# Kernel optimization log

Measured on AMD Instinct MI355X. Metric: run time of the kernel, lower is better.

## Reference

```python
import jax, jax.numpy as jnp
import numpy as np

N_NODES = 20000
N_EDGES = 640000
NUM_FEATURES = 128
HIDDEN = 64
HEADS = 4
NUM_CLASSES = 16
NEG_SLOPE = 0.2  # PyG GATConv default leaky_relu slope


def gat_conv(x, src, dst, W, att_s, att_d, b, num_nodes, concat):
    """PyG-style GATConv (inference: attention dropout is identity).
    x: [N, F_in]; src/dst: [E] (self-loops already included);
    W: [F_in, H*C]; att_s/att_d: [H, C]; b: [H*C] or [C]."""
    H, C = att_s.shape
    h = (x @ W).reshape(num_nodes, H, C)            # [N,H,C]
    a_s = jnp.sum(h * att_s, axis=-1)               # [N,H]
    a_d = jnp.sum(h * att_d, axis=-1)               # [N,H]
    e = jax.nn.leaky_relu(a_s[src] + a_d[dst], NEG_SLOPE)  # [E,H]
    # softmax over incoming edges of each destination node
    emax = jax.ops.segment_max(e, dst, num_segments=num_nodes)  # [N,H]
    ex = jnp.exp(e - emax[dst])
    denom = jax.ops.segment_sum(ex, dst, num_segments=num_nodes)
    alpha = ex / denom[dst]                         # [E,H]
    msg = h[src] * alpha[..., None]                 # [E,H,C]
    out = jax.ops.segment_sum(msg, dst, num_segments=num_nodes)  # [N,H,C]
    out = out.reshape(num_nodes, H * C) if concat else out.mean(axis=1)
    return out + b


def setup_inputs() -> dict:
    key = jax.random.key(0)
    ks = jax.random.split(key, 12)
    d1_in, d1_out = NUM_FEATURES, HEADS * HIDDEN
    d2_in, d2_out = HEADS * HIDDEN, HEADS * HIDDEN
    return {
        "x": jax.random.normal(ks[0], (N_NODES, NUM_FEATURES), dtype=jnp.float32),
        "edge_index": jax.random.randint(ks[1], (2, N_EDGES), 0, N_NODES, dtype=jnp.int64)
        if jax.config.jax_enable_x64 else
        jax.random.randint(ks[1], (2, N_EDGES), 0, N_NODES, dtype=jnp.int32),
        "W1": jax.random.normal(ks[2], (d1_in, d1_out), dtype=jnp.float32) / np.sqrt(d1_in),
        "att_src1": jax.random.normal(ks[3], (HEADS, HIDDEN), dtype=jnp.float32) / np.sqrt(HIDDEN),
        "att_dst1": jax.random.normal(ks[4], (HEADS, HIDDEN), dtype=jnp.float32) / np.sqrt(HIDDEN),
        "b1": jnp.zeros((HEADS * HIDDEN,), dtype=jnp.float32),
        "W2": jax.random.normal(ks[5], (d2_in, d2_out), dtype=jnp.float32) / np.sqrt(d2_in),
        "att_src2": jax.random.normal(ks[6], (HEADS, HIDDEN), dtype=jnp.float32) / np.sqrt(HIDDEN),
        "att_dst2": jax.random.normal(ks[7], (HEADS, HIDDEN), dtype=jnp.float32) / np.sqrt(HIDDEN),
        "b2": jnp.zeros((HIDDEN,), dtype=jnp.float32),
        "Wout": jax.random.normal(ks[8], (HIDDEN, NUM_CLASSES), dtype=jnp.float32) / np.sqrt(HIDDEN),
        "bout": jnp.zeros((NUM_CLASSES,), dtype=jnp.float32),
    }


def reference(x, edge_index, W1, att_src1, att_dst1, b1, W2, att_src2, att_dst2, b2, Wout, bout):
    N = x.shape[0]
    loops = jnp.arange(N, dtype=edge_index.dtype)
    src = jnp.concatenate([edge_index[0], loops])   # PyG add_self_loops=True
    dst = jnp.concatenate([edge_index[1], loops])
    h = gat_conv(x, src, dst, W1, att_src1, att_dst1, b1, N, concat=True)
    h = jax.nn.elu(h)                               # dropout is identity at eval
    h = gat_conv(h, src, dst, W2, att_src2, att_dst2, b2, N, concat=False)
    return h @ Wout + bout
```

## Files before the change

### kernel.cpp

```cpp
#include <hip/hip_runtime.h>
#include <hip/hip_bf16.h>
#include <hip/hip_fp16.h>


#define HEADS 4
#define CDIM 64
#define HC 256
#define ELLW 96
#define CNTS 16
#define NCHUNK 320

typedef __attribute__((ext_vector_type(8))) short bf16x8;
typedef __attribute__((ext_vector_type(4))) float f32x4;

__device__ __forceinline__ short f32_to_bf16_rne(float v) {
  unsigned u = __float_as_uint(v);
  unsigned r = (u + 0x7FFFu + ((u >> 16) & 1u)) >> 16;
  return (short)r;
}
__device__ __forceinline__ float bf16_bits_to_f32(short s) {
  return __uint_as_float(((unsigned)(unsigned short)s) << 16);
}

__device__ __forceinline__ void fma_mix2(float& alo, float& ahi,
                                         unsigned reg, float ex) {
  asm("v_fma_mix_f32 %0, %2, %3, %0 op_sel:[0,0,0] op_sel_hi:[1,0,0]\n\t"
      "v_fma_mix_f32 %1, %2, %3, %1 op_sel:[1,0,0] op_sel_hi:[1,0,0]"
      : "+v"(alo), "+v"(ahi)
      : "v"(reg), "v"(ex));
}

__global__ __launch_bounds__(256) void pack_w12_kernel(
    const float* __restrict__ W1, short* __restrict__ W1h,
    short* __restrict__ W1l, const float* __restrict__ W2,
    short* __restrict__ W2h, short* __restrict__ W2l,
    int* __restrict__ cnt, int N) {
  const int i = blockIdx.x * 256 + threadIdx.x;
  if (i < N) cnt[i * CNTS] = 0;
  if (i < 128 * 256) {
    const int k = i >> 8, n = i & 255;
    const float v = W1[i];
    const short hi = f32_to_bf16_rne(v);
    W1h[n * 128 + k] = hi;
    W1l[n * 128 + k] = f32_to_bf16_rne(v - bf16_bits_to_f32(hi));
  } else {
    const int j = i - 128 * 256;
    if (j >= 256 * 256) return;
    const int k = j >> 8, n = j & 255;
    const float v = W2[j];
    const short hi = f32_to_bf16_rne(v);
    W2h[n * 256 + k] = hi;
    W2l[n * 256 + k] = f32_to_bf16_rne(v - bf16_bits_to_f32(hi));
  }
}

__global__ __launch_bounds__(128) void gemm_mfma_split(
    const float* __restrict__ A, const short* __restrict__ Wt_hi,
    const short* __restrict__ Wt_lo, __half* __restrict__ h16,
    const float* __restrict__ att_s, const float* __restrict__ att_d,
    float* __restrict__ a_s, float* __restrict__ a_d, int M, int K) {
  __shared__ alignas(16) short As_hi[64 * 32];
  __shared__ alignas(16) short As_lo[64 * 32];
  const int t = threadIdx.x;
  const int wave = t >> 6;
  const int lane = t & 63;
  const int quad = lane >> 4;
  const int m16 = lane & 15;
  const int row0 = blockIdx.x * 64;
  const int col0 = blockIdx.y * 128 + wave * 64;
  const int head = col0 >> 6;

  f32x4 acc[4][4] = {};

  for (int k0 = 0; k0 < K; k0 += 32) {
    if (k0) __syncthreads();
#pragma unroll
    for (int uu = 0; uu < 2; ++uu) {
      const int u = t + uu * 128;
      const int r = u >> 2, seg = u & 3;
      const int gr = row0 + r;
      float vv[8] = {0.f, 0.f, 0.f, 0.f, 0.f, 0.f, 0.f, 0.f};
      if (gr < M) {
        const float* ap = A + (size_t)gr * K + k0 + seg * 8;
        const float4 v0 = *(const float4*)ap;
        const float4 v1 = *(const float4*)(ap + 4);
        vv[0] = v0.x; vv[1] = v0.y; vv[2] = v0.z; vv[3] = v0.w;
        vv[4] = v1.x; vv[5] = v1.y; vv[6] = v1.z; vv[7] = v1.w;
      }
      bf16x8 h8, l8;
#pragma unroll
      for (int j = 0; j < 8; ++j) {
        const short hi = f32_to_bf16_rne(vv[j]);
        h8[j] = hi;
        l8[j] = f32_to_bf16_rne(vv[j] - bf16_bits_to_f32(hi));
      }
      *(bf16x8*)(As_hi + r * 32 + seg * 8) = h8;
      *(bf16x8*)(As_lo + r * 32 + seg * 8) = l8;
    }
    bf16x8 b_hi[4], b_lo[4];
#pragma unroll
    for (int nt = 0; nt < 4; ++nt) {
      const size_t off = (size_t)(col0 + nt * 16 + m16) * K + k0 + quad * 8;
      b_hi[nt] = *(const bf16x8*)(Wt_hi + off);
      b_lo[nt] = *(const bf16x8*)(Wt_lo + off);
    }
    __syncthreads();
    bf16x8 a_hi[4], a_lo[4];
#pragma unroll
    for (int mt = 0; mt < 4; ++mt) {
      const int off = (mt * 16 + m16) * 32 + quad * 8;
      a_hi[mt] = *(const bf16x8*)(As_hi + off);
      a_lo[mt] = *(const bf16x8*)(As_lo + off);
    }
#pragma unroll
    for (int mt = 0; mt < 4; ++mt)
#pragma unroll
      for (int nt = 0; nt < 4; ++nt) {
        acc[mt][nt] = __builtin_amdgcn_mfma_f32_16x16x32_bf16(
            a_hi[mt], b_hi[nt], acc[mt][nt], 0, 0, 0);
        acc[mt][nt] = __builtin_amdgcn_mfma_f32_16x16x32_bf16(
            a_hi[mt], b_lo[nt], acc[mt][nt], 0, 0, 0);
        acc[mt][nt] = __builtin_amdgcn_mfma_f32_16x16x32_bf16(
            a_lo[mt], b_hi[nt], acc[mt][nt], 0, 0, 0);
      }
  }
  float sa[4], da[4];
#pragma unroll
  for (int nt = 0; nt < 4; ++nt) {
    sa[nt] = att_s[col0 + nt * 16 + m16];
    da[nt] = att_d[col0 + nt * 16 + m16];
  }
#pragma unroll
  for (int mt = 0; mt < 4; ++mt)
#pragma unroll
    for (int r = 0; r < 4; ++r) {
      const int gr = row0 + mt * 16 + quad * 4 + r;
      float ps = acc[mt][0][r] * sa[0] + acc[mt][1][r] * sa[1] +
                 acc[mt][2][r] * sa[2] + acc[mt][3][r] * sa[3];
      float pd = acc[mt][0][r] * da[0] + acc[mt][1][r] * da[1] +
                 acc[mt][2][r] * da[2] + acc[mt][3][r] * da[3];
#pragma unroll
      for (int off = 1; off <= 8; off <<= 1) {
        ps += __shfl_xor(ps, off);
        pd += __shfl_xor(pd, off);
      }
      if (gr < M) {
        if (m16 == 0) {
          a_s[gr * HEADS + head] = ps;
          a_d[gr * HEADS + head] = pd;
        }
#pragma unroll
        for (int nt = 0; nt < 4; ++nt)
          h16[(size_t)gr * HC + col0 + nt * 16 + m16] =
              __float2half(acc[mt][nt][r]);
      }
    }
}

__global__ __launch_bounds__(256) void ell_scatter_kernel(
    const int* __restrict__ src, const int* __restrict__ dst,
    int* __restrict__ cnt, int* __restrict__ ell, int E_raw, int Etot,
    int chunk_sz) {
  const int g = blockIdx.x & 7;
  const int e0 = (blockIdx.x >> 3) * chunk_sz;
  int e1 = e0 + chunk_sz;
  if (e1 > Etot) e1 = Etot;
  for (int e = e0 + threadIdx.x; e < e1; e += 256) {
    const int d = (e < E_raw) ? dst[e] : (e - E_raw);
    if (((d >> 8) & 7) != g) continue;
    const int s = (e < E_raw) ? src[e] : (e - E_raw);
    const int pos = atomicAdd(&cnt[d * CNTS], 1);
    if (pos < ELLW) ell[d * ELLW + pos] = s;
  }
}

__global__ __launch_bounds__(256) void gat_aggregate_kernel(
    const int* __restrict__ cnt, const int* __restrict__ ell,
    const __half* __restrict__ h16, const float* __restrict__ a_s,
    const float* __restrict__ a_d, const float* __restrict__ b,
    float* __restrict__ out, int N, int mode) {
  const int nn = __builtin_amdgcn_readfirstlane(
      blockIdx.x * 4 + (threadIdx.x >> 6));
  if (nn >= N) return;
  const int lane = threadIdx.x & 63;
  const int hd = lane >> 4;
  const float ad = a_d[nn * HEADS + hd];
  const int deg = __builtin_amdgcn_readfirstlane(cnt[nn * CNTS]);
  const int* __restrict__ rowp = ell + nn * ELLW;
  const unsigned nclamp = (unsigned)(N - 1);
  const char* __restrict__ hby = (const char*)h16;
  const unsigned lo8 = (unsigned)lane * 8u;
  float acc0 = 0.f, acc1 = 0.f, acc2 = 0.f, acc3 = 0.f, den = 0.f;

  for (int j0 = 0; j0 < deg; j0 += 8) {
    unsigned su[8];
#pragma unroll
    for (int j = 0; j < 8; ++j) {
      const unsigned s = (unsigned)rowp[j0 + j];
      su[j] = (s > nclamp) ? nclamp : s;
    }
    float asv[8];
    uint2 hv[8];
#pragma unroll
    for (int j = 0; j < 8; ++j) {
      asv[j] = a_s[su[j] * HEADS + hd];
      hv[j] = *(const uint2*)(hby + (((size_t)su[j]) << 9) + lo8);
    }
#pragma unroll
    for (int j = 0; j < 8; ++j) {
      float a = asv[j] + ad;
      a = fmaxf(a, 0.2f * a);
      const float ex = (j0 + j < deg) ? __expf(a) : 0.f;
      den += ex;
      fma_mix2(acc0, acc1, hv[j].x, ex);
      fma_mix2(acc2, acc3, hv[j].y, ex);
    }
  }

  const float inv = 1.f / den;
  float u0 = acc0 * inv, u1 = acc1 * inv, u2 = acc2 * inv, u3 = acc3 * inv;
  if (mode == 0) {
    const float4 bb = *(const float4*)(b + lane * 4);
    u0 += bb.x; u1 += bb.y; u2 += bb.z; u3 += bb.w;
    u0 = (u0 > 0.f) ? u0 : (__expf(u0) - 1.f);
    u1 = (u1 > 0.f) ? u1 : (__expf(u1) - 1.f);
    u2 = (u2 > 0.f) ? u2 : (__expf(u2) - 1.f);
    u3 = (u3 > 0.f) ? u3 : (__expf(u3) - 1.f);
  }
  *(float4*)(out + (size_t)nn * HC + lane * 4) = make_float4(u0, u1, u2, u3);
}

__global__ __launch_bounds__(256) void final_fused_kernel(
    const float* __restrict__ agg, const float* __restrict__ b2,
    const float* __restrict__ Wout, const float* __restrict__ bout,
    float* __restrict__ out, int N) {
  const int n = blockIdx.x * 4 + (threadIdx.x >> 6);
  const int c = threadIdx.x & 63;
  if (n >= N) return;
  const float* ar = agg + (size_t)n * HC;
  const float m = 0.25f * (ar[c] + ar[c + 64] + ar[c + 128] + ar[c + 192]) +
                  b2[c];
  const float4* wr = (const float4*)(Wout + c * 16);
  const float4 w0 = wr[0], w1 = wr[1], w2 = wr[2], w3 = wr[3];
  float p[16] = {m * w0.x, m * w0.y, m * w0.z, m * w0.w,
                 m * w1.x, m * w1.y, m * w1.z, m * w1.w,
                 m * w2.x, m * w2.y, m * w2.z, m * w2.w,
                 m * w3.x, m * w3.y, m * w3.z, m * w3.w};
#pragma unroll
  for (int off = 1; off < 64; off <<= 1)
#pragma unroll
    for (int j = 0; j < 16; ++j) p[j] += __shfl_xor(p[j], off);
  if (c == 0) {
    float* op = out + (size_t)n * 16;
    *(float4*)op = make_float4(p[0] + bout[0], p[1] + bout[1],
                               p[2] + bout[2], p[3] + bout[3]);
    *(float4*)(op + 4) = make_float4(p[4] + bout[4], p[5] + bout[5],
                                     p[6] + bout[6], p[7] + bout[7]);
    *(float4*)(op + 8) = make_float4(p[8] + bout[8], p[9] + bout[9],
                                     p[10] + bout[10], p[11] + bout[11]);
    *(float4*)(op + 12) = make_float4(p[12] + bout[12], p[13] + bout[13],
                                      p[14] + bout[14], p[15] + bout[15]);
  }
}

extern "C" void kernel_launch(void* const* d_in, const int* in_sizes, int n_in,
                              void* d_out, int out_size, void* d_ws, size_t ws_size,
                              hipStream_t stream) {
  const float* x      = (const float*)d_in[0];
  const int*   eidx   = (const int*)d_in[1];
  const float* W1     = (const float*)d_in[2];
  const float* att_s1 = (const float*)d_in[3];
  const float* att_d1 = (const float*)d_in[4];
  const float* b1     = (const float*)d_in[5];
  const float* W2     = (const float*)d_in[6];
  const float* att_s2 = (const float*)d_in[7];
  const float* att_d2 = (const float*)d_in[8];
  const float* b2     = (const float*)d_in[9];
  const float* Wout   = (const float*)d_in[10];
  const float* bout   = (const float*)d_in[11];
  float* out          = (float*)d_out;

  const int N     = in_sizes[0] / 128;
  const int E_raw = in_sizes[1] / 2;
  const int Etot  = E_raw + N;
  const int* src = eidx;
  const int* dst = eidx + E_raw;

  float* ws = (float*)d_ws;
  float* buf_agg = ws;
  float* buf_as  = buf_agg + (size_t)N * HC;
  float* buf_ad  = buf_as + (size_t)N * HEADS;
  __half* h16    = (__half*)(buf_ad + (size_t)N * HEADS);
  int* cnt  = (int*)(h16 + (size_t)N * HC);
  int* ell  = cnt + (size_t)N * CNTS;
  uintptr_t wp = ((uintptr_t)(ell + (size_t)N * ELLW) + 15) & ~(uintptr_t)15;
  short* wt1_hi = (short*)wp;
  short* wt1_lo = wt1_hi + 256 * 128;
  short* wt2_hi = wt1_lo + 256 * 128;
  short* wt2_lo = wt2_hi + 256 * 256;

  const dim3 blk(256);
  const int chunk_sz = (Etot + NCHUNK - 1) / NCHUNK;
  const dim3 g_gemm((N + 63) / 64, 2);
  const dim3 blk_gemm(128);
  const int g_agg = (N + 3) / 4;

  pack_w12_kernel<<<(384 * 256 + 255) / 256, blk, 0, stream>>>(
      W1, wt1_hi, wt1_lo, W2, wt2_hi, wt2_lo, cnt, N);
  ell_scatter_kernel<<<NCHUNK * 8, blk, 0, stream>>>(src, dst, cnt, ell,
                                                     E_raw, Etot, chunk_sz);

  gemm_mfma_split<<<g_gemm, blk_gemm, 0, stream>>>(
      x, wt1_hi, wt1_lo, h16, att_s1, att_d1, buf_as, buf_ad, N, 128);
  gat_aggregate_kernel<<<g_agg, blk, 0, stream>>>(cnt, ell, h16, buf_as,
                                                  buf_ad, b1, buf_agg, N, 0);

  gemm_mfma_split<<<g_gemm, blk_gemm, 0, stream>>>(
      buf_agg, wt2_hi, wt2_lo, h16, att_s2, att_d2, buf_as, buf_ad, N, 256);
  gat_aggregate_kernel<<<g_agg, blk, 0, stream>>>(cnt, ell, h16, buf_as,
                                                  buf_ad, b2, buf_agg, N, 1);

  final_fused_kernel<<<(N + 3) / 4, blk, 0, stream>>>(buf_agg, b2, Wout, bout,
                                                      out, N);
}
```

Measured before the change: 257.3 us.

## Store features head-major and split aggregation across heads per block

The GEMM epilogue now writes the fp16 features in a head-major layout, one [N,64] slice per head. The aggregation kernel launches four times as many blocks, and each block handles a single head. Within a wave, the two half-waves each take alternate neighbours, loading 4 bytes per lane from a compact 128-byte row, then combine their partial sums with a cross-half shuffle. The aim is to shrink each block's gather working set, with the cost of 4x redundant index and attention-score loads and half the lanes idle at write-out.

After: 365.0 us. 1.42x slower.

```diff
diff --git a/kernel.cpp b/kernel.cpp
--- a/kernel.cpp
+++ b/kernel.cpp
@@ -130,6 +130,7 @@
     sa[nt] = att_s[col0 + nt * 16 + m16];
     da[nt] = att_d[col0 + nt * 16 + m16];
   }
+  __half* __restrict__ hsl = h16 + (size_t)head * M * CDIM;
 #pragma unroll
   for (int mt = 0; mt < 4; ++mt)
 #pragma unroll
@@ -151,7 +152,7 @@
         }
 #pragma unroll
         for (int nt = 0; nt < 4; ++nt)
-          h16[(size_t)gr * HC + col0 + nt * 16 + m16] =
+          hsl[(size_t)gr * CDIM + nt * 16 + m16] =
               __float2half(acc[mt][nt][r]);
       }
     }
@@ -179,18 +180,22 @@
     const __half* __restrict__ h16, const float* __restrict__ a_s,
     const float* __restrict__ a_d, const float* __restrict__ b,
     float* __restrict__ out, int N, int mode) {
+  const int bid = blockIdx.x;
+  const int hd = bid & 3;
   const int nn = __builtin_amdgcn_readfirstlane(
-      blockIdx.x * 4 + (threadIdx.x >> 6));
+      (bid >> 2) * 4 + (threadIdx.x >> 6));
   if (nn >= N) return;
   const int lane = threadIdx.x & 63;
-  const int hd = lane >> 4;
+  const int half = lane >> 5;
+  const int ch2 = (lane & 31) * 2;
   const float ad = a_d[nn * HEADS + hd];
   const int deg = __builtin_amdgcn_readfirstlane(cnt[nn * CNTS]);
   const int* __restrict__ rowp = ell + nn * ELLW;
   const unsigned nclamp = (unsigned)(N - 1);
-  const char* __restrict__ hby = (const char*)h16;
-  const unsigned lo8 = (unsigned)lane * 8u;
-  float acc0 = 0.f, acc1 = 0.f, acc2 = 0.f, acc3 = 0.f, den = 0.f;
+  const char* __restrict__ hsl =
+      (const char*)h16 + (size_t)hd * N * (CDIM * 2);
+  const unsigned choff = (unsigned)(ch2 * 2);
+  float accL = 0.f, accH = 0.f, den = 0.f;
 
   for (int j0 = 0; j0 < deg; j0 += 8) {
     unsigned su[8];
@@ -200,34 +205,36 @@
       su[j] = (s > nclamp) ? nclamp : s;
     }
     float asv[8];
-    uint2 hv[8];
-#pragma unroll
-    for (int j = 0; j < 8; ++j) {
-      asv[j] = a_s[su[j] * HEADS + hd];
-      hv[j] = *(const uint2*)(hby + (((size_t)su[j]) << 9) + lo8);
-    }
-#pragma unroll
-    for (int j = 0; j < 8; ++j) {
+#pragma unroll
+    for (int j = 0; j < 8; ++j) asv[j] = a_s[su[j] * HEADS + hd];
+    unsigned hv[4];
+#pragma unroll
+    for (int k = 0; k < 4; ++k)
+      hv[k] = *(const unsigned*)(hsl + ((size_t)su[2 * k + half] << 7) + choff);
+#pragma unroll
+    for (int k = 0; k < 4; ++k) {
+      const int j = 2 * k + half;
       float a = asv[j] + ad;
       a = fmaxf(a, 0.2f * a);
       const float ex = (j0 + j < deg) ? __expf(a) : 0.f;
       den += ex;
-      fma_mix2(acc0, acc1, hv[j].x, ex);
-      fma_mix2(acc2, acc3, hv[j].y, ex);
-    }
-  }
-
-  const float inv = 1.f / den;
-  float u0 = acc0 * inv, u1 = acc1 * inv, u2 = acc2 * inv, u3 = acc3 * inv;
-  if (mode == 0) {
-    const float4 bb = *(const float4*)(b + lane * 4);
-    u0 += bb.x; u1 += bb.y; u2 += bb.z; u3 += bb.w;
-    u0 = (u0 > 0.f) ? u0 : (__expf(u0) - 1.f);
-    u1 = (u1 > 0.f) ? u1 : (__expf(u1) - 1.f);
-    u2 = (u2 > 0.f) ? u2 : (__expf(u2) - 1.f);
-    u3 = (u3 > 0.f) ? u3 : (__expf(u3) - 1.f);
-  }
-  *(float4*)(out + (size_t)nn * HC + lane * 4) = make_float4(u0, u1, u2, u3);
+      fma_mix2(accL, accH, hv[k], ex);
+    }
+  }
+  den += __shfl_xor(den, 32);
+  accL += __shfl_xor(accL, 32);
+  accH += __shfl_xor(accH, 32);
+  if (half == 0) {
+    const float inv = 1.f / den;
+    float u0 = accL * inv, u1 = accH * inv;
+    if (mode == 0) {
+      const float2 bb = *(const float2*)(b + hd * CDIM + ch2);
+      u0 += bb.x; u1 += bb.y;
+      u0 = (u0 > 0.f) ? u0 : (__expf(u0) - 1.f);
+      u1 = (u1 > 0.f) ? u1 : (__expf(u1) - 1.f);
+    }
+    *(float2*)(out + (size_t)nn * HC + hd * CDIM + ch2) = make_float2(u0, u1);
+  }
 }
 
 __global__ __launch_bounds__(256) void final_fused_kernel(
@@ -303,7 +310,7 @@
   const int chunk_sz = (Etot + NCHUNK - 1) / NCHUNK;
   const dim3 g_gemm((N + 63) / 64, 2);
   const dim3 blk_gemm(128);
-  const int g_agg = (N + 3) / 4;
+  const int g_agg = ((N + 3) / 4) * 4;
 
   pack_w12_kernel<<<(384 * 256 + 255) / 256, blk, 0, stream>>>(
       W1, wt1_hi, wt1_lo, W2, wt2_hi, wt2_lo, cnt, N);
```
